# Performance work log

Hardware: AMD Instinct MI355X
Metric: run time of the kernel (lower is better)

The kernel has to match this reference:

```python
import jax, jax.numpy as jnp
import numpy as np

BN_EPS = 1e-5


def setup_inputs() -> dict:
    key = jax.random.key(0)
    ks = jax.random.split(key, 12)
    B, N, S, D1, D2 = 8, 8192, 2048, 128, 256
    C_in = D2 + D1  # 384
    mlp = [256, 128]
    inp = {
        "xyz1": jax.random.normal(ks[0], (B, 3, N), jnp.float32),
        "xyz2": jax.random.normal(ks[1], (B, 3, S), jnp.float32),
        "points1": jax.random.normal(ks[2], (B, D1, N), jnp.float32),
        "points2": jax.random.normal(ks[3], (B, D2, S), jnp.float32),
    }
    # conv0: in 384 -> 256, conv1: 256 -> 128 (1x1 Conv1d == per-point matmul)
    inp["w0"] = jax.random.normal(ks[4], (mlp[0], C_in), jnp.float32) * (1.0 / np.sqrt(C_in))
    inp["b0"] = jax.random.normal(ks[5], (mlp[0],), jnp.float32) * 0.01
    inp["g0"] = jnp.ones((mlp[0],), jnp.float32)
    inp["be0"] = jnp.zeros((mlp[0],), jnp.float32)
    inp["w1"] = jax.random.normal(ks[6], (mlp[1], mlp[0]), jnp.float32) * (1.0 / np.sqrt(mlp[0]))
    inp["b1"] = jax.random.normal(ks[7], (mlp[1],), jnp.float32) * 0.01
    inp["g1"] = jnp.ones((mlp[1],), jnp.float32)
    inp["be1"] = jnp.zeros((mlp[1],), jnp.float32)
    return inp


def _conv_bn_relu(x, w, b, g, be):
    # 1x1 Conv1d + BatchNorm1d (training-mode batch stats, biased var) + ReLU
    x = jnp.einsum("oc,bcn->bon", w, x) + b[None, :, None]
    m = jnp.mean(x, axis=(0, 2), keepdims=True)
    v = jnp.var(x, axis=(0, 2), keepdims=True)
    x = (x - m) * jax.lax.rsqrt(v + BN_EPS) * g[None, :, None] + be[None, :, None]
    return jax.nn.relu(x)


def reference(xyz1, xyz2, points1, points2, w0, b0, g0, be0, w1, b1, g1, be1):
    B, _, N = xyz1.shape
    S = xyz2.shape[2]
    src = jnp.transpose(xyz1, (0, 2, 1))  # [B,N,3]
    dst = jnp.transpose(xyz2, (0, 2, 1))  # [B,S,3]
    # squared pairwise distance [B,N,S]
    dist = (
        jnp.sum(src * src, axis=-1)[:, :, None]
        + jnp.sum(dst * dst, axis=-1)[:, None, :]
        - 2.0 * jnp.einsum("bnc,bsc->bns", src, dst)
    )
    # 3 nearest neighbors (smallest dist, sorted)
    neg_d, idx = jax.lax.top_k(-dist, 3)  # [B,N,3]
    d3 = -neg_d
    recip = 1.0 / (d3 + 1e-8)
    weight = recip / jnp.sum(recip, axis=-1, keepdims=True)  # [B,N,3]
    p2t = jnp.transpose(points2, (0, 2, 1))  # [B,S,D']
    gathered = jnp.take_along_axis(
        p2t, idx.reshape(B, N * 3)[:, :, None], axis=1
    ).reshape(B, N, 3, -1)  # [B,N,3,D']
    interp = jnp.einsum("bnkd,bnk->bdn", gathered, weight)  # [B,D',N]
    x = jnp.concatenate([interp, points1], axis=1)  # [B,D'+D,N]
    x = _conv_bn_relu(x, w0, b0, g0, be0)
    x = _conv_bn_relu(x, w1, b1, g1, be1)
    return x
```

## Files before the change

### kernel.cpp

```cpp
#include <hip/hip_runtime.h>
#include <hip/hip_bf16.h>

constexpr int kB = 8, kN = 8192, kS = 2048;
constexpr int kD1 = 128, kD2 = 256, kCin = 384, kM0 = 256, kM1 = 128;
constexpr float kEps = 1e-5f;

typedef float f32x4 __attribute__((ext_vector_type(4)));
typedef short bf16x8 __attribute__((ext_vector_type(8)));
typedef unsigned short u16x4 __attribute__((ext_vector_type(4)));

__device__ inline unsigned short f2bf(float f) {
    __hip_bfloat16 h = __float2bfloat16(f);
    return *reinterpret_cast<unsigned short*>(&h);
}
__device__ inline float bf2f(unsigned short u) {
    unsigned int v = (unsigned int)u << 16;
    return *reinterpret_cast<float*>(&v);
}

__global__ __launch_bounds__(256) void transpose_p2_kernel(
    const float* __restrict__ in, float* __restrict__ out)
{
    __shared__ float tl[64][69];
    const int s0 = blockIdx.x * 64, c0 = blockIdx.y * 64, b = blockIdx.z;
    const int t = threadIdx.x;
    const int rlo = t >> 4, rhi = t & 15;
#pragma unroll
    for (int r = 0; r < 4; ++r) {
        const int cl = rlo + r * 16;
        f32x4 v = *(const f32x4*)(in + ((size_t)(b * kD2 + c0 + cl)) * kS + s0 + rhi * 4);
#pragma unroll
        for (int j = 0; j < 4; ++j) tl[cl][rhi * 4 + j] = v[j];
    }
    __syncthreads();
#pragma unroll
    for (int r = 0; r < 4; ++r) {
        const int sl = rlo + r * 16;
        f32x4 v;
#pragma unroll
        for (int j = 0; j < 4; ++j) v[j] = tl[rhi * 4 + j][sl];
        *(f32x4*)(out + ((size_t)(b * kS + s0 + sl)) * kD2 + c0 + rhi * 4) = v;
    }
}

__global__ __launch_bounds__(256) void transpose_p1_kernel(
    const float* __restrict__ in, unsigned short* __restrict__ xt)
{
    __shared__ float tl[64][69];
    const int n0 = blockIdx.x * 64, c0 = blockIdx.y * 64, b = blockIdx.z;
    const int t = threadIdx.x;
    const int rlo = t >> 4, rhi = t & 15;
#pragma unroll
    for (int r = 0; r < 4; ++r) {
        const int cl = rlo + r * 16;
        f32x4 v = *(const f32x4*)(in + ((size_t)(b * kD1 + c0 + cl)) * kN + n0 + rhi * 4);
#pragma unroll
        for (int j = 0; j < 4; ++j) tl[cl][rhi * 4 + j] = v[j];
    }
    __syncthreads();
#pragma unroll
    for (int r = 0; r < 4; ++r) {
        const int nl = rlo + r * 16;
        u16x4 u;
#pragma unroll
        for (int j = 0; j < 4; ++j) u[j] = f2bf(tl[rhi * 4 + j][nl]);
        *(u16x4*)(xt + ((size_t)(b * kN + n0 + nl)) * kCin + 256 + c0 + rhi * 4) = u;
    }
}

__global__ __launch_bounds__(256) void knn_interp_kernel(
    const float* __restrict__ xyz1, const float* __restrict__ xyz2,
    const float* __restrict__ p2t, unsigned short* __restrict__ xt)
{
    __shared__ f32x4 sp[kS];
    const int b = blockIdx.x >> 7;
    const int n0 = (blockIdx.x & 127) << 6;
    const int t = threadIdx.x;
    const float* x2 = xyz2 + b * 3 * kS;
    for (int s = t; s < kS; s += 256) {
        float sx = x2[s], sy = x2[kS + s], sz = x2[2 * kS + s];
        f32x4 q = {sx, sy, sz, fmaf(sx, sx, fmaf(sy, sy, sz * sz))};
        sp[s] = q;
    }
    __syncthreads();
    const int q = t >> 2, c = t & 3;
    const int n = n0 + q;
    const float* x1 = xyz1 + b * 3 * kN;
    const float px = x1[n], py = x1[kN + n], pz = x1[2 * kN + n];
    const float ax = -2.f * px, ay = -2.f * py, az = -2.f * pz;

    float a0 = 1e30f, a1 = 1e30f, a2 = 1e30f;
    float c0v = 1e30f, c1v = 1e30f, c2v = 1e30f;
    for (int i = 0; i < 512; i += 2) {
        f32x4 qa = sp[4 * i + c];
        f32x4 qb = sp[4 * i + 4 + c];
        float e0 = fmaf(ax, qa[0], fmaf(ay, qa[1], fmaf(az, qa[2], qa[3])));
        float e1 = fmaf(ax, qb[0], fmaf(ay, qb[1], fmaf(az, qb[2], qb[3])));
        float t1 = __builtin_amdgcn_fmed3f(e0, a0, a1);
        float t2 = __builtin_amdgcn_fmed3f(e0, a1, a2);
        a0 = fminf(a0, e0); a1 = t1; a2 = t2;
        t1 = __builtin_amdgcn_fmed3f(e1, c0v, c1v);
        t2 = __builtin_amdgcn_fmed3f(e1, c1v, c2v);
        c0v = fminf(c0v, e1); c1v = t1; c2v = t2;
    }
    float x0 = fminf(a0, c0v);
    float x1v = fminf(fmaxf(a0, c0v), fminf(a1, c1v));
    float x2v = fminf(fminf(fmaxf(a1, c0v), fmaxf(a0, c1v)), fminf(a2, c2v));
#pragma unroll
    for (int off = 1; off <= 2; off <<= 1) {
        float y0 = __shfl_xor(x0, off), y1 = __shfl_xor(x1v, off), y2 = __shfl_xor(x2v, off);
        float z0 = fminf(x0, y0);
        float z1 = fminf(fmaxf(x0, y0), fminf(x1v, y1));
        float z2 = fminf(fminf(fmaxf(x1v, y0), fmaxf(x0, y1)), fminf(x2v, y2));
        x0 = z0; x1v = z1; x2v = z2;
    }
    const float cutoff = x2v + 1e-3f;

    double d0 = 1e300, d1 = 1e300, d2 = 1e300;
    int i0 = 0, i1 = 0, i2 = 0;
    const double dpx = (double)px, dpy = (double)py, dpz = (double)pz;
    for (int i = 0; i < 512; ++i) {
        const int s = 4 * i + c;
        f32x4 qv = sp[s];
        float df = fmaf(ax, qv[0], fmaf(ay, qv[1], fmaf(az, qv[2], qv[3])));
        if (df <= cutoff) {
            double ex = dpx - (double)qv[0], ey = dpy - (double)qv[1], ez = dpz - (double)qv[2];
            double d = ex * ex + ey * ey + ez * ez;
            if (d < d2) {
                if (d < d1) {
                    if (d < d0) { d2 = d1; i2 = i1; d1 = d0; i1 = i0; d0 = d; i0 = s; }
                    else        { d2 = d1; i2 = i1; d1 = d;  i1 = s; }
                } else          { d2 = d;  i2 = s; }
            }
        }
    }
#pragma unroll
    for (int off = 1; off <= 2; off <<= 1) {
        double pd0 = __shfl_xor(d0, off), pd1 = __shfl_xor(d1, off), pd2 = __shfl_xor(d2, off);
        int pi0 = __shfl_xor(i0, off), pi1 = __shfl_xor(i1, off), pi2 = __shfl_xor(i2, off);
#pragma unroll
        for (int m = 0; m < 3; ++m) {
            double pd = (m == 0) ? pd0 : (m == 1) ? pd1 : pd2;
            int pi = (m == 0) ? pi0 : (m == 1) ? pi1 : pi2;
            if (pd < d2 || (pd == d2 && pi < i2)) {
                if (pd < d1 || (pd == d1 && pi < i1)) {
                    if (pd < d0 || (pd == d0 && pi < i0)) {
                        d2 = d1; i2 = i1; d1 = d0; i1 = i0; d0 = pd; i0 = pi;
                    } else { d2 = d1; i2 = i1; d1 = pd; i1 = pi; }
                } else { d2 = pd; i2 = pi; }
            }
        }
    }
    const double r0 = 1.0 / (d0 + 1e-8), r1 = 1.0 / (d1 + 1e-8), r2 = 1.0 / (d2 + 1e-8);
    const double rs = 1.0 / (r0 + r1 + r2);
    const float w0 = (float)(r0 * rs), w1 = (float)(r1 * rs), w2 = (float)(r2 * rs);

    const f32x4* row0 = (const f32x4*)(p2t + ((size_t)(b * kS) + i0) * kD2);
    const f32x4* row1 = (const f32x4*)(p2t + ((size_t)(b * kS) + i1) * kD2);
    const f32x4* row2 = (const f32x4*)(p2t + ((size_t)(b * kS) + i2) * kD2);
    unsigned short* dst = xt + ((size_t)(b * kN) + n) * kCin;
#pragma unroll 4
    for (int j = 0; j < 16; ++j) {
        const int ch = c + 4 * j;
        f32x4 v = w0 * row0[ch] + w1 * row1[ch] + w2 * row2[ch];
        u16x4 u = {f2bf(v[0]), f2bf(v[1]), f2bf(v[2]), f2bf(v[3])};
        *(u16x4*)(dst + ch * 4) = u;
    }
}

__device__ inline int swz(int row, int ks) {
    return row * 32 + ((ks ^ ((row >> 1) & 3)) << 3);
}

template <int K, int MTOT, bool BNRELU, bool OUTBF16>
__global__ __launch_bounds__(256) void gemm_bn_kernel(
    const float* __restrict__ W, const unsigned short* __restrict__ X,
    const float* __restrict__ scale, const float* __restrict__ shift,
    unsigned short* __restrict__ Yb, float* __restrict__ Yf,
    float* __restrict__ gsum, float* __restrict__ gsq)
{
    constexpr int BM = 128, BN = 128;
    __shared__ unsigned short Al[BM * 32], Bl[BN * 32];
    __shared__ float ssum[BM], ssq[BM];
    __shared__ float s_sc[256], s_sh[256];
    const int t = threadIdx.x;
    const int bn = blockIdx.x * BN, bo = blockIdx.y * BM, b = blockIdx.z;
    const int l = t & 63, w = t >> 6;
    const int wm = (w >> 1) * 64, wn = (w & 1) * 64;
    const int lrow = l & 15, lks = l >> 4;

    if constexpr (BNRELU) {
        if (t < K) { s_sc[t] = scale[t]; s_sh[t] = shift[t]; }
    }
    if (t < BM) { ssum[t] = 0.f; ssq[t] = 0.f; }
    __syncthreads();

    f32x4 acc[4][4] = {};
    for (int k0 = 0; k0 < K; k0 += 32) {
#pragma unroll
        for (int r = 0; r < 2; ++r) {
            const int sid = t + r * 256;
            const int m = sid >> 2, ks = sid & 3;
            const float* wp = W + (size_t)(bo + m) * K + k0 + ks * 8;
            f32x4 wa = *(const f32x4*)wp, wb = *(const f32x4*)(wp + 4);
            bf16x8 u;
#pragma unroll
            for (int j = 0; j < 4; ++j) { u[j] = (short)f2bf(wa[j]); u[j + 4] = (short)f2bf(wb[j]); }
            *(bf16x8*)(Al + swz(m, ks)) = u;
        }
#pragma unroll
        for (int r = 0; r < 2; ++r) {
            const int sid = t + r * 256;
            const int nl = sid >> 2, ks = sid & 3;
            bf16x8 v = *(const bf16x8*)(X + ((size_t)(b * kN) + bn + nl) * K + k0 + ks * 8);
            if constexpr (BNRELU) {
#pragma unroll
                for (int j = 0; j < 8; ++j) {
                    const int ch = k0 + ks * 8 + j;
                    float f = fmaxf(fmaf(bf2f((unsigned short)v[j]), s_sc[ch], s_sh[ch]), 0.f);
                    v[j] = (short)f2bf(f);
                }
            }
            *(bf16x8*)(Bl + swz(nl, ks)) = v;
        }
        __syncthreads();
        bf16x8 af[4], bfr[4];
#pragma unroll
        for (int f = 0; f < 4; ++f) af[f]  = *(const bf16x8*)(Al + swz(wm + f * 16 + lrow, lks));
#pragma unroll
        for (int f = 0; f < 4; ++f) bfr[f] = *(const bf16x8*)(Bl + swz(wn + f * 16 + lrow, lks));
#pragma unroll
        for (int mi = 0; mi < 4; ++mi)
#pragma unroll
            for (int ni = 0; ni < 4; ++ni)
                acc[mi][ni] = __builtin_amdgcn_mfma_f32_16x16x32_bf16(af[mi], bfr[ni], acc[mi][ni], 0, 0, 0);
        __syncthreads();
    }

#pragma unroll
    for (int mi = 0; mi < 4; ++mi) {
#pragma unroll
        for (int r = 0; r < 4; ++r) {
            float ps = 0.f, pq = 0.f;
#pragma unroll
            for (int ni = 0; ni < 4; ++ni) { float v = acc[mi][ni][r]; ps += v; pq += v * v; }
#pragma unroll
            for (int off = 1; off < 16; off <<= 1) { ps += __shfl_xor(ps, off); pq += __shfl_xor(pq, off); }
            if (lrow == 0) {
                const int m = wm + mi * 16 + lks * 4 + r;
                atomicAdd(&ssum[m], ps); atomicAdd(&ssq[m], pq);
            }
        }
    }

    if constexpr (OUTBF16) {
#pragma unroll
        for (int mi = 0; mi < 4; ++mi)
#pragma unroll
            for (int ni = 0; ni < 4; ++ni) {
                const int m = bo + wm + mi * 16 + lks * 4;
                const int n = bn + wn + ni * 16 + lrow;
                u16x4 u = {f2bf(acc[mi][ni][0]), f2bf(acc[mi][ni][1]),
                           f2bf(acc[mi][ni][2]), f2bf(acc[mi][ni][3])};
                *(u16x4*)(Yb + ((size_t)(b * kN) + n) * MTOT + m) = u;
            }
    } else {
#pragma unroll
        for (int mi = 0; mi < 4; ++mi)
#pragma unroll
            for (int ni = 0; ni < 4; ++ni) {
                const int n = bn + wn + ni * 16 + lrow;
#pragma unroll
                for (int r = 0; r < 4; ++r) {
                    const int m = bo + wm + mi * 16 + lks * 4 + r;
                    Yf[((size_t)(b * MTOT) + m) * kN + n] = acc[mi][ni][r];
                }
            }
    }
    __syncthreads();
    if (t < BM) {
        atomicAdd(&gsum[bo + t], ssum[t]);
        atomicAdd(&gsq[bo + t], ssq[t]);
    }
}

__global__ void bn_finalize_kernel(const float* __restrict__ gsum, const float* __restrict__ gsq,
                                   const float* __restrict__ g, const float* __restrict__ be,
                                   float* __restrict__ scale, float* __restrict__ shift, int M)
{
    int t = threadIdx.x;
    if (t < M) {
        const float invn = 1.0f / 65536.0f;
        float mean = gsum[t] * invn;
        float var = gsq[t] * invn - mean * mean;
        float sc = g[t] * rsqrtf(var + kEps);
        scale[t] = sc;
        shift[t] = fmaf(-mean, sc, be[t]);
    }
}

__global__ __launch_bounds__(256) void bn_relu_out_kernel(
    float* __restrict__ out, const float* __restrict__ scale, const float* __restrict__ shift)
{
    const int total = kB * kM1 * kN / 4;
    for (int idx = blockIdx.x * blockDim.x + threadIdx.x; idx < total;
         idx += gridDim.x * blockDim.x) {
        const int p = (idx >> 11) & 127;
        const float sc = scale[p], sh = shift[p];
        f32x4 v = ((f32x4*)out)[idx];
#pragma unroll
        for (int j = 0; j < 4; ++j) v[j] = fmaxf(fmaf(v[j], sc, sh), 0.f);
        ((f32x4*)out)[idx] = v;
    }
}

extern "C" void kernel_launch(void* const* d_in, const int* in_sizes, int n_in,
                              void* d_out, int out_size, void* d_ws, size_t ws_size,
                              hipStream_t stream)
{
    const float* xyz1    = (const float*)d_in[0];
    const float* xyz2    = (const float*)d_in[1];
    const float* points1 = (const float*)d_in[2];
    const float* points2 = (const float*)d_in[3];
    const float* w0      = (const float*)d_in[4];
    const float* g0      = (const float*)d_in[6];
    const float* be0     = (const float*)d_in[7];
    const float* w1      = (const float*)d_in[8];
    const float* g1      = (const float*)d_in[10];
    const float* be1     = (const float*)d_in[11];
    float* out = (float*)d_out;

    char* ws = (char*)d_ws;
    unsigned short* xt  = (unsigned short*)ws;
    float* p2t          = (float*)(ws + (size_t)50331648);
    unsigned short* y0t = (unsigned short*)(ws + (size_t)67108864);
    float* stats        = (float*)(ws + (size_t)100663296);
    float* sum0 = stats,          *sq0 = stats + 256;
    float* sum1 = stats + 512,    *sq1 = stats + 640;
    float* scale0 = stats + 768,  *shift0 = stats + 1024;
    float* scale1 = stats + 1280, *shift1 = stats + 1408;

    hipMemsetAsync(stats, 0, 768 * sizeof(float), stream);
    transpose_p2_kernel<<<dim3(32, 4, 8), 256, 0, stream>>>(points2, p2t);
    transpose_p1_kernel<<<dim3(128, 2, 8), 256, 0, stream>>>(points1, xt);
    knn_interp_kernel<<<1024, 256, 0, stream>>>(xyz1, xyz2, p2t, xt);
    gemm_bn_kernel<kCin, kM0, false, true><<<dim3(64, 2, 8), 256, 0, stream>>>(
        w0, xt, nullptr, nullptr, y0t, nullptr, sum0, sq0);
    bn_finalize_kernel<<<1, 256, 0, stream>>>(sum0, sq0, g0, be0, scale0, shift0, 256);
    gemm_bn_kernel<kM0, kM1, true, false><<<dim3(64, 1, 8), 256, 0, stream>>>(
        w1, y0t, scale0, shift0, nullptr, out, sum1, sq1);
    bn_finalize_kernel<<<1, 128, 0, stream>>>(sum1, sq1, g1, be1, scale1, shift1, 128);
    bn_relu_out_kernel<<<2048, 256, 0, stream>>>(out, scale1, shift1);
}
```

Measured before the change: 182.9 us.

## Recompute second GEMM for output BN instead of storing, halve KNN lanes per query

The second 1x1-conv GEMM now runs twice. The first pass only accumulates BatchNorm statistics and writes nothing. The second pass recomputes the GEMM and applies the final BN+ReLU in its epilogue, which removes the fp32 write of the pre-BN output and the separate read-modify-write pass over it. Separately, the KNN kernel uses 2 lanes per query point instead of 4, with 128 points per block and 512 blocks, and the unrolled scan loop has one running top-3 instead of two. This trades redundant GEMM arithmetic and fewer KNN blocks for less memory traffic and fewer shuffle stages.

After: 233.6 us. +27.7%, slower.

```diff
diff --git a/kernel.cpp b/kernel.cpp
--- a/kernel.cpp
+++ b/kernel.cpp
@@ -73,8 +73,8 @@
     const float* __restrict__ p2t, unsigned short* __restrict__ xt)
 {
     __shared__ f32x4 sp[kS];
-    const int b = blockIdx.x >> 7;
-    const int n0 = (blockIdx.x & 127) << 6;
+    const int b = blockIdx.x >> 6;
+    const int n0 = (blockIdx.x & 63) << 7;
     const int t = threadIdx.x;
     const float* x2 = xyz2 + b * 3 * kS;
     for (int s = t; s < kS; s += 256) {
@@ -83,61 +83,56 @@
         sp[s] = q;
     }
     __syncthreads();
-    const int q = t >> 2, c = t & 3;
+    const int q = t >> 1, par = t & 1;
     const int n = n0 + q;
     const float* x1 = xyz1 + b * 3 * kN;
     const float px = x1[n], py = x1[kN + n], pz = x1[2 * kN + n];
     const float ax = -2.f * px, ay = -2.f * py, az = -2.f * pz;
 
     float a0 = 1e30f, a1 = 1e30f, a2 = 1e30f;
-    float c0v = 1e30f, c1v = 1e30f, c2v = 1e30f;
-    for (int i = 0; i < 512; i += 2) {
-        f32x4 qa = sp[4 * i + c];
-        f32x4 qb = sp[4 * i + 4 + c];
-        float e0 = fmaf(ax, qa[0], fmaf(ay, qa[1], fmaf(az, qa[2], qa[3])));
-        float e1 = fmaf(ax, qb[0], fmaf(ay, qb[1], fmaf(az, qb[2], qb[3])));
-        float t1 = __builtin_amdgcn_fmed3f(e0, a0, a1);
-        float t2 = __builtin_amdgcn_fmed3f(e0, a1, a2);
-        a0 = fminf(a0, e0); a1 = t1; a2 = t2;
-        t1 = __builtin_amdgcn_fmed3f(e1, c0v, c1v);
-        t2 = __builtin_amdgcn_fmed3f(e1, c1v, c2v);
-        c0v = fminf(c0v, e1); c1v = t1; c2v = t2;
-    }
-    float x0 = fminf(a0, c0v);
-    float x1v = fminf(fmaxf(a0, c0v), fminf(a1, c1v));
-    float x2v = fminf(fminf(fmaxf(a1, c0v), fmaxf(a0, c1v)), fminf(a2, c2v));
-#pragma unroll
-    for (int off = 1; off <= 2; off <<= 1) {
-        float y0 = __shfl_xor(x0, off), y1 = __shfl_xor(x1v, off), y2 = __shfl_xor(x2v, off);
-        float z0 = fminf(x0, y0);
-        float z1 = fminf(fmaxf(x0, y0), fminf(x1v, y1));
-        float z2 = fminf(fminf(fmaxf(x1v, y0), fmaxf(x0, y1)), fminf(x2v, y2));
-        x0 = z0; x1v = z1; x2v = z2;
-    }
-    const float cutoff = x2v + 1e-3f;
+    for (int i = 0; i < 1024; i += 8) {
+#pragma unroll
+        for (int j = 0; j < 8; ++j) {
+            f32x4 qv = sp[2 * (i + j) + par];
+            float e = fmaf(ax, qv[0], fmaf(ay, qv[1], fmaf(az, qv[2], qv[3])));
+            float t1 = __builtin_amdgcn_fmed3f(e, a0, a1);
+            float t2 = __builtin_amdgcn_fmed3f(e, a1, a2);
+            a0 = fminf(a0, e); a1 = t1; a2 = t2;
+        }
+    }
+    {
+        float y0 = __shfl_xor(a0, 1), y1 = __shfl_xor(a1, 1), y2 = __shfl_xor(a2, 1);
+        float z0 = fminf(a0, y0);
+        float z1 = fminf(fmaxf(a0, y0), fminf(a1, y1));
+        float z2 = fminf(fminf(fmaxf(a1, y0), fmaxf(a0, y1)), fminf(a2, y2));
+        a0 = z0; a1 = z1; a2 = z2;
+    }
+    const float cutoff = a2 + 1e-3f;
 
     double d0 = 1e300, d1 = 1e300, d2 = 1e300;
     int i0 = 0, i1 = 0, i2 = 0;
     const double dpx = (double)px, dpy = (double)py, dpz = (double)pz;
-    for (int i = 0; i < 512; ++i) {
-        const int s = 4 * i + c;
-        f32x4 qv = sp[s];
-        float df = fmaf(ax, qv[0], fmaf(ay, qv[1], fmaf(az, qv[2], qv[3])));
-        if (df <= cutoff) {
-            double ex = dpx - (double)qv[0], ey = dpy - (double)qv[1], ez = dpz - (double)qv[2];
-            double d = ex * ex + ey * ey + ez * ez;
-            if (d < d2) {
-                if (d < d1) {
-                    if (d < d0) { d2 = d1; i2 = i1; d1 = d0; i1 = i0; d0 = d; i0 = s; }
-                    else        { d2 = d1; i2 = i1; d1 = d;  i1 = s; }
-                } else          { d2 = d;  i2 = s; }
-            }
-        }
-    }
-#pragma unroll
-    for (int off = 1; off <= 2; off <<= 1) {
-        double pd0 = __shfl_xor(d0, off), pd1 = __shfl_xor(d1, off), pd2 = __shfl_xor(d2, off);
-        int pi0 = __shfl_xor(i0, off), pi1 = __shfl_xor(i1, off), pi2 = __shfl_xor(i2, off);
+    for (int i = 0; i < 1024; i += 2) {
+#pragma unroll
+        for (int j = 0; j < 2; ++j) {
+            const int s = 2 * (i + j) + par;
+            f32x4 qv = sp[s];
+            float df = fmaf(ax, qv[0], fmaf(ay, qv[1], fmaf(az, qv[2], qv[3])));
+            if (df <= cutoff) {
+                double ex = dpx - (double)qv[0], ey = dpy - (double)qv[1], ez = dpz - (double)qv[2];
+                double d = ex * ex + ey * ey + ez * ez;
+                if (d < d2) {
+                    if (d < d1) {
+                        if (d < d0) { d2 = d1; i2 = i1; d1 = d0; i1 = i0; d0 = d; i0 = s; }
+                        else        { d2 = d1; i2 = i1; d1 = d;  i1 = s; }
+                    } else          { d2 = d;  i2 = s; }
+                }
+            }
+        }
+    }
+    {
+        double pd0 = __shfl_xor(d0, 1), pd1 = __shfl_xor(d1, 1), pd2 = __shfl_xor(d2, 1);
+        int pi0 = __shfl_xor(i0, 1), pi1 = __shfl_xor(i1, 1), pi2 = __shfl_xor(i2, 1);
 #pragma unroll
         for (int m = 0; m < 3; ++m) {
             double pd = (m == 0) ? pd0 : (m == 1) ? pd1 : pd2;
@@ -160,8 +155,8 @@
     const f32x4* row2 = (const f32x4*)(p2t + ((size_t)(b * kS) + i2) * kD2);
     unsigned short* dst = xt + ((size_t)(b * kN) + n) * kCin;
 #pragma unroll 4
-    for (int j = 0; j < 16; ++j) {
-        const int ch = c + 4 * j;
+    for (int j = 0; j < 32; ++j) {
+        const int ch = par + 2 * j;
         f32x4 v = w0 * row0[ch] + w1 * row1[ch] + w2 * row2[ch];
         u16x4 u = {f2bf(v[0]), f2bf(v[1]), f2bf(v[2]), f2bf(v[3])};
         *(u16x4*)(dst + ch * 4) = u;
@@ -172,17 +167,19 @@
     return row * 32 + ((ks ^ ((row >> 1) & 3)) << 3);
 }
 
-template <int K, int MTOT, bool BNRELU, bool OUTBF16>
+template <int K, int MTOT, bool BNRELU, int OUTMODE, bool STATS>
 __global__ __launch_bounds__(256) void gemm_bn_kernel(
     const float* __restrict__ W, const unsigned short* __restrict__ X,
     const float* __restrict__ scale, const float* __restrict__ shift,
+    const float* __restrict__ scaleO, const float* __restrict__ shiftO,
     unsigned short* __restrict__ Yb, float* __restrict__ Yf,
     float* __restrict__ gsum, float* __restrict__ gsq)
 {
     constexpr int BM = 128, BN = 128;
     __shared__ unsigned short Al[BM * 32], Bl[BN * 32];
     __shared__ float ssum[BM], ssq[BM];
-    __shared__ float s_sc[256], s_sh[256];
+    __shared__ float s_sc[K > 0 ? K : 1], s_sh[K > 0 ? K : 1];
+    __shared__ float s_scO[BM], s_shO[BM];
     const int t = threadIdx.x;
     const int bn = blockIdx.x * BN, bo = blockIdx.y * BM, b = blockIdx.z;
     const int l = t & 63, w = t >> 6;
@@ -192,7 +189,12 @@
     if constexpr (BNRELU) {
         if (t < K) { s_sc[t] = scale[t]; s_sh[t] = shift[t]; }
     }
-    if (t < BM) { ssum[t] = 0.f; ssq[t] = 0.f; }
+    if constexpr (OUTMODE == 3) {
+        if (t < BM) { s_scO[t] = scaleO[bo + t]; s_shO[t] = shiftO[bo + t]; }
+    }
+    if constexpr (STATS) {
+        if (t < BM) { ssum[t] = 0.f; ssq[t] = 0.f; }
+    }
     __syncthreads();
 
     f32x4 acc[4][4] = {};
@@ -237,23 +239,25 @@
         __syncthreads();
     }
 
-#pragma unroll
-    for (int mi = 0; mi < 4; ++mi) {
-#pragma unroll
-        for (int r = 0; r < 4; ++r) {
-            float ps = 0.f, pq = 0.f;
-#pragma unroll
-            for (int ni = 0; ni < 4; ++ni) { float v = acc[mi][ni][r]; ps += v; pq += v * v; }
-#pragma unroll
-            for (int off = 1; off < 16; off <<= 1) { ps += __shfl_xor(ps, off); pq += __shfl_xor(pq, off); }
-            if (lrow == 0) {
-                const int m = wm + mi * 16 + lks * 4 + r;
-                atomicAdd(&ssum[m], ps); atomicAdd(&ssq[m], pq);
-            }
-        }
-    }
-
-    if constexpr (OUTBF16) {
+    if constexpr (STATS) {
+#pragma unroll
+        for (int mi = 0; mi < 4; ++mi) {
+#pragma unroll
+            for (int r = 0; r < 4; ++r) {
+                float ps = 0.f, pq = 0.f;
+#pragma unroll
+                for (int ni = 0; ni < 4; ++ni) { float v = acc[mi][ni][r]; ps += v; pq += v * v; }
+#pragma unroll
+                for (int off = 1; off < 16; off <<= 1) { ps += __shfl_xor(ps, off); pq += __shfl_xor(pq, off); }
+                if (lrow == 0) {
+                    const int m = wm + mi * 16 + lks * 4 + r;
+                    atomicAdd(&ssum[m], ps); atomicAdd(&ssq[m], pq);
+                }
+            }
+        }
+    }
+
+    if constexpr (OUTMODE == 0) {
 #pragma unroll
         for (int mi = 0; mi < 4; ++mi)
 #pragma unroll
@@ -264,7 +268,7 @@
                            f2bf(acc[mi][ni][2]), f2bf(acc[mi][ni][3])};
                 *(u16x4*)(Yb + ((size_t)(b * kN) + n) * MTOT + m) = u;
             }
-    } else {
+    } else if constexpr (OUTMODE == 3) {
 #pragma unroll
         for (int mi = 0; mi < 4; ++mi)
 #pragma unroll
@@ -272,15 +276,18 @@
                 const int n = bn + wn + ni * 16 + lrow;
 #pragma unroll
                 for (int r = 0; r < 4; ++r) {
-                    const int m = bo + wm + mi * 16 + lks * 4 + r;
-                    Yf[((size_t)(b * MTOT) + m) * kN + n] = acc[mi][ni][r];
+                    const int ml = wm + mi * 16 + lks * 4 + r;
+                    float v = fmaxf(fmaf(acc[mi][ni][r], s_scO[ml], s_shO[ml]), 0.f);
+                    Yf[((size_t)(b * MTOT) + bo + ml) * kN + n] = v;
                 }
             }
     }
-    __syncthreads();
-    if (t < BM) {
-        atomicAdd(&gsum[bo + t], ssum[t]);
-        atomicAdd(&gsq[bo + t], ssq[t]);
+    if constexpr (STATS) {
+        __syncthreads();
+        if (t < BM) {
+            atomicAdd(&gsum[bo + t], ssum[t]);
+            atomicAdd(&gsq[bo + t], ssq[t]);
+        }
     }
 }
 
@@ -296,21 +303,6 @@
         float sc = g[t] * rsqrtf(var + kEps);
         scale[t] = sc;
         shift[t] = fmaf(-mean, sc, be[t]);
-    }
-}
-
-__global__ __launch_bounds__(256) void bn_relu_out_kernel(
-    float* __restrict__ out, const float* __restrict__ scale, const float* __restrict__ shift)
-{
-    const int total = kB * kM1 * kN / 4;
-    for (int idx = blockIdx.x * blockDim.x + threadIdx.x; idx < total;
-         idx += gridDim.x * blockDim.x) {
-        const int p = (idx >> 11) & 127;
-        const float sc = scale[p], sh = shift[p];
-        f32x4 v = ((f32x4*)out)[idx];
-#pragma unroll
-        for (int j = 0; j < 4; ++j) v[j] = fmaxf(fmaf(v[j], sc, sh), 0.f);
-        ((f32x4*)out)[idx] = v;
     }
 }
 
@@ -343,12 +335,13 @@
     hipMemsetAsync(stats, 0, 768 * sizeof(float), stream);
     transpose_p2_kernel<<<dim3(32, 4, 8), 256, 0, stream>>>(points2, p2t);
     transpose_p1_kernel<<<dim3(128, 2, 8), 256, 0, stream>>>(points1, xt);
-    knn_interp_kernel<<<1024, 256, 0, stream>>>(xyz1, xyz2, p2t, xt);
-    gemm_bn_kernel<kCin, kM0, false, true><<<dim3(64, 2, 8), 256, 0, stream>>>(
-        w0, xt, nullptr, nullptr, y0t, nullptr, sum0, sq0);
+    knn_interp_kernel<<<512, 256, 0, stream>>>(xyz1, xyz2, p2t, xt);
+    gemm_bn_kernel<kCin, kM0, false, 0, true><<<dim3(64, 2, 8), 256, 0, stream>>>(
+        w0, xt, nullptr, nullptr, nullptr, nullptr, y0t, nullptr, sum0, sq0);
     bn_finalize_kernel<<<1, 256, 0, stream>>>(sum0, sq0, g0, be0, scale0, shift0, 256);
-    gemm_bn_kernel<kM0, kM1, true, false><<<dim3(64, 1, 8), 256, 0, stream>>>(
-        w1, y0t, scale0, shift0, nullptr, out, sum1, sq1);
+    gemm_bn_kernel<kM0, kM1, true, 2, true><<<dim3(64, 1, 8), 256, 0, stream>>>(
+        w1, y0t, scale0, shift0, nullptr, nullptr, nullptr, nullptr, sum1, sq1);
     bn_finalize_kernel<<<1, 128, 0, stream>>>(sum1, sq1, g1, be1, scale1, shift1, 128);
-    bn_relu_out_kernel<<<2048, 256, 0, stream>>>(out, scale1, shift1);
-}
+    gemm_bn_kernel<kM0, kM1, true, 3, false><<<dim3(64, 1, 8), 256, 0, stream>>>(
+        w1, y0t, scale0, shift0, scale1, shift1, nullptr, out, nullptr, nullptr);
+}
```
